# Optimization experiments

Measured on AMD Instinct MI355X. Metric: run time of the kernel, lower is better.

## Reference

```python
import jax, jax.numpy as jnp
import numpy as np

T, D_MODEL, D_FF, N_EXPERTS, TOP_K = 8192, 1024, 4096, 8, 2

def setup_inputs() -> dict:
    key = jax.random.key(0)
    k1, k2, k3, k4, k5 = jax.random.split(key, 5)
    hidden_states = jax.random.normal(k1, (T, D_MODEL), dtype=jnp.float32)
    # router picks TOP_K distinct-ish experts per token; build one-hot mask [T, K, E]
    expert_idx = jax.random.randint(k2, (T, TOP_K), 0, N_EXPERTS)
    selected_experts = jax.nn.one_hot(expert_idx, N_EXPERTS, dtype=jnp.int32)
    rw = jax.random.uniform(k3, (T, TOP_K), dtype=jnp.float32)
    routing_weights = rw / jnp.sum(rw, axis=-1, keepdims=True)
    scale = 1.0 / np.sqrt(D_MODEL)
    wi = jax.random.normal(k4, (N_EXPERTS, D_FF, D_MODEL), dtype=jnp.float32) * scale
    wo = jax.random.normal(k5, (N_EXPERTS, D_MODEL, D_FF), dtype=jnp.float32) * (1.0 / np.sqrt(D_FF))
    return {"hidden_states": hidden_states, "selected_experts": selected_experts,
            "routing_weights": routing_weights, "wi": wi, "wo": wo}

def reference(hidden_states, selected_experts, routing_weights, wi, wo):
    # expert_mask: [E, K, T] (as in torch permute(2,1,0))
    mask = jnp.transpose(selected_experts, (2, 1, 0)).astype(hidden_states.dtype)
    # combined per-token weight for each expert: w[t, e] = sum_k mask[e,k,t]*routing_weights[t,k]
    w = jnp.einsum('ekt,tk->te', mask, routing_weights)
    out = jnp.zeros_like(hidden_states)
    # fixed small loop over experts; tokens not routed to expert e get weight 0,
    # so this is mathematically identical to the gather->MLP->scale->scatter-add.
    for e in range(wi.shape[0]):
        h = jax.nn.relu(hidden_states @ wi[e].T)     # [T, d_ff] (dropout is identity at eval)
        y = h @ wo[e].T                              # [T, d_model]
        out = out + w[:, e:e + 1] * y
    return out
```

## Files before the change

kernel.cpp:

```cpp
#include <hip/hip_runtime.h>
#include <hip/hip_bf16.h>


#define T_TOK   8192
#define D_MODEL 1024
#define D_FF    4096
#define NE      8
#define MT2     72
#define ROWS_MAX (MT2 * 256)
#define BUFB    32768
#define LDS_G1  98304
#define BUF2    24576
#define LDS_G2  73728

typedef float f32x4 __attribute__((ext_vector_type(4)));
typedef short s16x8 __attribute__((ext_vector_type(8)));
typedef short s16x4 __attribute__((ext_vector_type(4)));
typedef unsigned short u16;

__device__ __forceinline__ u16 f2bf(float x) {
  __hip_bfloat16 h = __float2bfloat16(x);
  return *reinterpret_cast<u16*>(&h);
}

__device__ __forceinline__ s16x8 cvt8(float4 a, float4 b) {
  s16x8 v;
  v[0] = (short)f2bf(a.x); v[1] = (short)f2bf(a.y);
  v[2] = (short)f2bf(a.z); v[3] = (short)f2bf(a.w);
  v[4] = (short)f2bf(b.x); v[5] = (short)f2bf(b.y);
  v[6] = (short)f2bf(b.z); v[7] = (short)f2bf(b.w);
  return v;
}

__device__ __forceinline__ void gload_lds16(const void* g, void* l) {
  __builtin_amdgcn_global_load_lds((const __attribute__((address_space(1))) void*)g,
                                   (__attribute__((address_space(3))) void*)l,
                                   16, 0, 0);
}

__global__ void moe_route(const int* __restrict__ sel, const float* __restrict__ rw,
                          int* __restrict__ cnt, int* __restrict__ tidx,
                          float* __restrict__ tw) {
  int t = blockIdx.x * blockDim.x + threadIdx.x;
  if (t >= T_TOK) return;
  int e0 = 0, e1 = 0;
  #pragma unroll
  for (int e = 0; e < NE; ++e) {
    if (sel[t * 16 + e])     e0 = e;
    if (sel[t * 16 + 8 + e]) e1 = e;
  }
  float w0 = rw[2 * t], w1 = rw[2 * t + 1];
  if (e0 == e1) {
    int p = atomicAdd(&cnt[e0], 1);
    tidx[e0 * T_TOK + p] = t; tw[e0 * T_TOK + p] = w0 + w1;
  } else {
    int p = atomicAdd(&cnt[e0], 1);
    tidx[e0 * T_TOK + p] = t; tw[e0 * T_TOK + p] = w0;
    int q = atomicAdd(&cnt[e1], 1);
    tidx[e1 * T_TOK + q] = t; tw[e1 * T_TOK + q] = w1;
  }
}

__global__ void moe_tilemap(const int* __restrict__ cnt, const int* __restrict__ tidx,
                            const float* __restrict__ tw, int* __restrict__ te256,
                            int* __restrict__ tokr, float* __restrict__ wr) {
  int off[NE + 1];
  {
    int o = 0;
    #pragma unroll
    for (int e = 0; e < NE; ++e) { off[e] = o; o += (cnt[e] + 255) & ~255; }
    off[NE] = o;
  }
  const int total = off[NE];
  const int gid = blockIdx.x * blockDim.x + threadIdx.x;
  const int stride = gridDim.x * blockDim.x;
  for (int t = gid; t < MT2; t += stride) {
    int r0 = t * 256; int e = -1;
    if (r0 < total) {
      #pragma unroll
      for (int i = NE - 1; i >= 0; --i) if (r0 >= off[i]) { e = i; break; }
    }
    te256[t] = e;
  }
  for (int i = gid; i < ROWS_MAX; i += stride) {
    if (i >= total) { tokr[i] = -1; wr[i] = 0.f; continue; }
    int e = 0;
    #pragma unroll
    for (int k = NE - 1; k >= 0; --k) if (i >= off[k]) { e = k; break; }
    int j = i - off[e];
    int ok = j < cnt[e];
    tokr[i] = ok ? tidx[e * T_TOK + j] : -1;
    wr[i]   = ok ? tw[e * T_TOK + j] : 0.f;
  }
}

__global__ void moe_gather_x(const float* __restrict__ hs, const int* __restrict__ tokr,
                             u16* __restrict__ Xg) {
  int row = blockIdx.x;
  int tok = tokr[row];
  int c = threadIdx.x * 4;
  u16* dst = Xg + (size_t)row * D_MODEL + c;
  s16x4 o;
  if (tok < 0) {
    o[0] = o[1] = o[2] = o[3] = 0;
  } else {
    float4 v = *(const float4*)(hs + (size_t)tok * D_MODEL + c);
    o[0] = (short)f2bf(v.x); o[1] = (short)f2bf(v.y);
    o[2] = (short)f2bf(v.z); o[3] = (short)f2bf(v.w);
  }
  *(s16x4*)dst = o;
}

__global__ void moe_cvt_w(const float* __restrict__ wi, const float* __restrict__ wo,
                          u16* __restrict__ wib, u16* __restrict__ wob) {
  const size_t NW = (size_t)NE * D_FF * D_MODEL;
  size_t i = ((size_t)blockIdx.x * blockDim.x + threadIdx.x) * 8;
  const float* src; u16* dst;
  if (i < NW) { src = wi + i; dst = wib + i; }
  else        { src = wo + (i - NW); dst = wob + (i - NW); }
  float4 a = *(const float4*)(src);
  float4 b = *(const float4*)(src + 4);
  *(s16x8*)dst = cvt8(a, b);
}

__global__ void moe_cvt_wi_s(const float* __restrict__ wi, u16* __restrict__ wis,
                             int W, int f0) {
  size_t i = ((size_t)blockIdx.x * blockDim.x + threadIdx.x) * 8;
  size_t per = (size_t)W * D_MODEL;
  int e = (int)(i / per); size_t r = i % per;
  const float* src = wi + ((size_t)e * D_FF + f0) * D_MODEL + r;
  float4 a = *(const float4*)src;
  float4 b = *(const float4*)(src + 4);
  *(s16x8*)(wis + i) = cvt8(a, b);
}

__global__ void moe_cvt_wo_s(const float* __restrict__ wo, u16* __restrict__ wos,
                             int W, int f0) {
  size_t i = ((size_t)blockIdx.x * blockDim.x + threadIdx.x) * 8;
  size_t per = (size_t)D_MODEL * W;
  int e = (int)(i / per); size_t r = i % per;
  int row = (int)(r / W), col = (int)(r % W);
  const float* src = wo + ((size_t)e * D_MODEL + row) * D_FF + f0 + col;
  float4 a = *(const float4*)src;
  float4 b = *(const float4*)(src + 4);
  *(s16x8*)(wos + i) = cvt8(a, b);
}

template <bool FULL>
__global__ __launch_bounds__(512, 1)
void moe_g1(const u16* __restrict__ Xg, const u16* __restrict__ wiP,
            const int* __restrict__ te256, u16* __restrict__ H,
            int W, int f0) {
  extern __shared__ char lds[];
  const int GR = gridDim.x;
  const int task = (blockIdx.x & 7) * (GR >> 3) + (blockIdx.x >> 3);
  const int mt = task % MT2;
  const int nc = task / MT2;
  const int e = te256[mt];
  if (e < 0) return;
  const int grow0 = mt * 256;
  const int fcol = nc * 256;

  const int tid = threadIdx.x;
  const int lane = tid & 63, wv = tid >> 6;
  const int lg = lane >> 4, ll = lane & 15;
  const int wm = wv >> 2, wn = wv & 3;

  const int sw = (tid * 16) ^ (((tid >> 3) & 7) << 4);
  const int srow = sw >> 6, scol = sw & 63;
  const int inner = (ll * 64 + lg * 16) ^ (((ll >> 1) & 7) << 4);

  const char* gA = (const char*)(Xg + (size_t)grow0 * D_MODEL);
  const char* gB = (const char*)(wiP + (FULL ? ((size_t)e * D_FF + f0 + fcol)
                                             : ((size_t)e * W + fcol)) * D_MODEL);

  f32x4 acc[8][4];
  #pragma unroll
  for (int m = 0; m < 8; ++m)
    #pragma unroll
    for (int n = 0; n < 4; ++n) acc[m][n] = (f32x4){0.f, 0.f, 0.f, 0.f};

  auto stage = [&](int kb, char* lbuf) {
    #pragma unroll
    for (int j = 0; j < 2; ++j)
      gload_lds16(gA + (size_t)(j * 128 + srow) * 2048 + kb + scol,
                  lbuf + j * 8192 + tid * 16);
    #pragma unroll
    for (int j = 0; j < 2; ++j)
      gload_lds16(gB + (size_t)(j * 128 + srow) * 2048 + kb + scol,
                  lbuf + 16384 + j * 8192 + tid * 16);
  };

  const int NT = D_MODEL / 32;
  stage(0, lds);
  stage(64, lds + BUFB);
  int bufi = 0;
  for (int t = 0; t < NT; ++t) {
    if (t < NT - 1) { asm volatile("s_waitcnt vmcnt(4)" ::: "memory"); }
    else            { asm volatile("s_waitcnt vmcnt(0)" ::: "memory"); }
    asm volatile("s_barrier" ::: "memory");
    const char* la = lds + bufi * BUFB + wm * 8192;
    const char* lb = lds + bufi * BUFB + 16384 + wn * 4096;
    if (t + 2 < NT) {
      int b2 = bufi + 2; if (b2 >= 3) b2 -= 3;
      stage((t + 2) * 64, lds + b2 * BUFB);
    }
    s16x8 bq0 = *(const s16x8*)(lb + 0 * 1024 + inner);
    s16x8 bq1 = *(const s16x8*)(lb + 1 * 1024 + inner);
    s16x8 bq2 = *(const s16x8*)(lb + 2 * 1024 + inner);
    s16x8 bq3 = *(const s16x8*)(lb + 3 * 1024 + inner);
    {
      s16x8 a0 = *(const s16x8*)(la + 0 * 1024 + inner);
      s16x8 a1 = *(const s16x8*)(la + 1 * 1024 + inner);
      s16x8 a2 = *(const s16x8*)(la + 2 * 1024 + inner);
      s16x8 a3 = *(const s16x8*)(la + 3 * 1024 + inner);
      __builtin_amdgcn_s_setprio(1);
      acc[0][0] = __builtin_amdgcn_mfma_f32_16x16x32_bf16(a0, bq0, acc[0][0], 0, 0, 0);
      acc[0][1] = __builtin_amdgcn_mfma_f32_16x16x32_bf16(a0, bq1, acc[0][1], 0, 0, 0);
      acc[0][2] = __builtin_amdgcn_mfma_f32_16x16x32_bf16(a0, bq2, acc[0][2], 0, 0, 0);
      acc[0][3] = __builtin_amdgcn_mfma_f32_16x16x32_bf16(a0, bq3, acc[0][3], 0, 0, 0);
      acc[1][0] = __builtin_amdgcn_mfma_f32_16x16x32_bf16(a1, bq0, acc[1][0], 0, 0, 0);
      acc[1][1] = __builtin_amdgcn_mfma_f32_16x16x32_bf16(a1, bq1, acc[1][1], 0, 0, 0);
      acc[1][2] = __builtin_amdgcn_mfma_f32_16x16x32_bf16(a1, bq2, acc[1][2], 0, 0, 0);
      acc[1][3] = __builtin_amdgcn_mfma_f32_16x16x32_bf16(a1, bq3, acc[1][3], 0, 0, 0);
      acc[2][0] = __builtin_amdgcn_mfma_f32_16x16x32_bf16(a2, bq0, acc[2][0], 0, 0, 0);
      acc[2][1] = __builtin_amdgcn_mfma_f32_16x16x32_bf16(a2, bq1, acc[2][1], 0, 0, 0);
      acc[2][2] = __builtin_amdgcn_mfma_f32_16x16x32_bf16(a2, bq2, acc[2][2], 0, 0, 0);
      acc[2][3] = __builtin_amdgcn_mfma_f32_16x16x32_bf16(a2, bq3, acc[2][3], 0, 0, 0);
      acc[3][0] = __builtin_amdgcn_mfma_f32_16x16x32_bf16(a3, bq0, acc[3][0], 0, 0, 0);
      acc[3][1] = __builtin_amdgcn_mfma_f32_16x16x32_bf16(a3, bq1, acc[3][1], 0, 0, 0);
      acc[3][2] = __builtin_amdgcn_mfma_f32_16x16x32_bf16(a3, bq2, acc[3][2], 0, 0, 0);
      acc[3][3] = __builtin_amdgcn_mfma_f32_16x16x32_bf16(a3, bq3, acc[3][3], 0, 0, 0);
      __builtin_amdgcn_s_setprio(0);
    }
    __builtin_amdgcn_s_barrier();
    {
      s16x8 a0 = *(const s16x8*)(la + 4 * 1024 + inner);
      s16x8 a1 = *(const s16x8*)(la + 5 * 1024 + inner);
      s16x8 a2 = *(const s16x8*)(la + 6 * 1024 + inner);
      s16x8 a3 = *(const s16x8*)(la + 7 * 1024 + inner);
      __builtin_amdgcn_s_setprio(1);
      acc[4][0] = __builtin_amdgcn_mfma_f32_16x16x32_bf16(a0, bq0, acc[4][0], 0, 0, 0);
      acc[4][1] = __builtin_amdgcn_mfma_f32_16x16x32_bf16(a0, bq1, acc[4][1], 0, 0, 0);
      acc[4][2] = __builtin_amdgcn_mfma_f32_16x16x32_bf16(a0, bq2, acc[4][2], 0, 0, 0);
      acc[4][3] = __builtin_amdgcn_mfma_f32_16x16x32_bf16(a0, bq3, acc[4][3], 0, 0, 0);
      acc[5][0] = __builtin_amdgcn_mfma_f32_16x16x32_bf16(a1, bq0, acc[5][0], 0, 0, 0);
      acc[5][1] = __builtin_amdgcn_mfma_f32_16x16x32_bf16(a1, bq1, acc[5][1], 0, 0, 0);
      acc[5][2] = __builtin_amdgcn_mfma_f32_16x16x32_bf16(a1, bq2, acc[5][2], 0, 0, 0);
      acc[5][3] = __builtin_amdgcn_mfma_f32_16x16x32_bf16(a1, bq3, acc[5][3], 0, 0, 0);
      acc[6][0] = __builtin_amdgcn_mfma_f32_16x16x32_bf16(a2, bq0, acc[6][0], 0, 0, 0);
      acc[6][1] = __builtin_amdgcn_mfma_f32_16x16x32_bf16(a2, bq1, acc[6][1], 0, 0, 0);
      acc[6][2] = __builtin_amdgcn_mfma_f32_16x16x32_bf16(a2, bq2, acc[6][2], 0, 0, 0);
      acc[6][3] = __builtin_amdgcn_mfma_f32_16x16x32_bf16(a2, bq3, acc[6][3], 0, 0, 0);
      acc[7][0] = __builtin_amdgcn_mfma_f32_16x16x32_bf16(a3, bq0, acc[7][0], 0, 0, 0);
      acc[7][1] = __builtin_amdgcn_mfma_f32_16x16x32_bf16(a3, bq1, acc[7][1], 0, 0, 0);
      acc[7][2] = __builtin_amdgcn_mfma_f32_16x16x32_bf16(a3, bq2, acc[7][2], 0, 0, 0);
      acc[7][3] = __builtin_amdgcn_mfma_f32_16x16x32_bf16(a3, bq3, acc[7][3], 0, 0, 0);
      __builtin_amdgcn_s_setprio(0);
    }
    bufi += 1; if (bufi >= 3) bufi -= 3;
  }

  #pragma unroll
  for (int mf = 0; mf < 8; ++mf) {
    #pragma unroll
    for (int r = 0; r < 4; ++r) {
      int row = grow0 + wm * 128 + mf * 16 + lg * 4 + r;
      u16* hp = H + (size_t)row * W + fcol + wn * 64 + ll;
      #pragma unroll
      for (int nf = 0; nf < 4; ++nf) {
        float v = acc[mf][nf][r];
        hp[nf * 16] = f2bf(v > 0.f ? v : 0.f);
      }
    }
  }
}

template <bool FULL>
__global__ __launch_bounds__(512, 4)
void moe_g2(const u16* __restrict__ H, const u16* __restrict__ woP,
            const int* __restrict__ te256, const int* __restrict__ tokr,
            const float* __restrict__ wr, float* __restrict__ out,
            int W, int f0, int KCH) {
  extern __shared__ char lds[];
  const int GR = gridDim.x;
  const int task = (blockIdx.x & 7) * (GR >> 3) + (blockIdx.x >> 3);
  const int dc = task & 7;
  const int rest = task >> 3;
  const int mt = rest % MT2;
  const int kc = rest / MT2;
  const int e = te256[mt];
  if (e < 0) return;
  const int grow0 = mt * 256;
  const int dcol0 = dc * 128;

  const int tid = threadIdx.x;
  const int lane = tid & 63, wv = tid >> 6;
  const int lg = lane >> 4, ll = lane & 15;
  const int wm = wv >> 1, wn = wv & 1;

  const int sw = (tid * 16) ^ (((tid >> 3) & 7) << 4);
  const int srow = sw >> 6, scol = sw & 63;
  const int inner = (ll * 64 + lg * 16) ^ (((ll >> 1) & 7) << 4);

  const size_t pA = (size_t)W * 2;
  const size_t pB = (FULL ? (size_t)D_FF : (size_t)W) * 2;
  const char* gA = (const char*)(H + (size_t)grow0 * W) + (size_t)kc * KCH * 2;
  const char* gB = (const char*)(woP + ((size_t)e * D_MODEL + dcol0) * (pB / 2)
                                 + (FULL ? f0 : 0)) + (size_t)kc * KCH * 2;

  f32x4 acc[4][4];
  #pragma unroll
  for (int m = 0; m < 4; ++m)
    #pragma unroll
    for (int n = 0; n < 4; ++n) acc[m][n] = (f32x4){0.f, 0.f, 0.f, 0.f};

  auto stage = [&](int kb, char* lbuf) {
    #pragma unroll
    for (int j = 0; j < 2; ++j)
      gload_lds16(gA + (size_t)(j * 128 + srow) * pA + kb + scol,
                  lbuf + j * 8192 + tid * 16);
    {
      int brow = srow & 127;
      gload_lds16(gB + (size_t)brow * pB + kb + ((sw & 8191) & 63)
                  , lbuf + 16384 + (tid & 511) * 16);
    }
  };

  const int NT = KCH / 32;
  stage(0, lds);
  stage(64, lds + BUF2);
  int bufi = 0;
  for (int t = 0; t < NT; ++t) {
    if (t < NT - 1) { asm volatile("s_waitcnt vmcnt(3)" ::: "memory"); }
    else            { asm volatile("s_waitcnt vmcnt(0)" ::: "memory"); }
    asm volatile("s_barrier" ::: "memory");
    const char* la = lds + bufi * BUF2 + wm * 4096;
    const char* lb = lds + bufi * BUF2 + 16384 + wn * 4096;
    if (t + 2 < NT) {
      int b2 = bufi + 2; if (b2 >= 3) b2 -= 3;
      stage((t + 2) * 64, lds + b2 * BUF2);
    }
    s16x8 bq0 = *(const s16x8*)(lb + 0 * 1024 + inner);
    s16x8 bq1 = *(const s16x8*)(lb + 1 * 1024 + inner);
    s16x8 bq2 = *(const s16x8*)(lb + 2 * 1024 + inner);
    s16x8 bq3 = *(const s16x8*)(lb + 3 * 1024 + inner);
    s16x8 a0 = *(const s16x8*)(la + 0 * 1024 + inner);
    s16x8 a1 = *(const s16x8*)(la + 1 * 1024 + inner);
    s16x8 a2 = *(const s16x8*)(la + 2 * 1024 + inner);
    s16x8 a3 = *(const s16x8*)(la + 3 * 1024 + inner);
    __builtin_amdgcn_s_setprio(1);
    acc[0][0] = __builtin_amdgcn_mfma_f32_16x16x32_bf16(a0, bq0, acc[0][0], 0, 0, 0);
    acc[0][1] = __builtin_amdgcn_mfma_f32_16x16x32_bf16(a0, bq1, acc[0][1], 0, 0, 0);
    acc[0][2] = __builtin_amdgcn_mfma_f32_16x16x32_bf16(a0, bq2, acc[0][2], 0, 0, 0);
    acc[0][3] = __builtin_amdgcn_mfma_f32_16x16x32_bf16(a0, bq3, acc[0][3], 0, 0, 0);
    acc[1][0] = __builtin_amdgcn_mfma_f32_16x16x32_bf16(a1, bq0, acc[1][0], 0, 0, 0);
    acc[1][1] = __builtin_amdgcn_mfma_f32_16x16x32_bf16(a1, bq1, acc[1][1], 0, 0, 0);
    acc[1][2] = __builtin_amdgcn_mfma_f32_16x16x32_bf16(a1, bq2, acc[1][2], 0, 0, 0);
    acc[1][3] = __builtin_amdgcn_mfma_f32_16x16x32_bf16(a1, bq3, acc[1][3], 0, 0, 0);
    acc[2][0] = __builtin_amdgcn_mfma_f32_16x16x32_bf16(a2, bq0, acc[2][0], 0, 0, 0);
    acc[2][1] = __builtin_amdgcn_mfma_f32_16x16x32_bf16(a2, bq1, acc[2][1], 0, 0, 0);
    acc[2][2] = __builtin_amdgcn_mfma_f32_16x16x32_bf16(a2, bq2, acc[2][2], 0, 0, 0);
    acc[2][3] = __builtin_amdgcn_mfma_f32_16x16x32_bf16(a2, bq3, acc[2][3], 0, 0, 0);
    acc[3][0] = __builtin_amdgcn_mfma_f32_16x16x32_bf16(a3, bq0, acc[3][0], 0, 0, 0);
    acc[3][1] = __builtin_amdgcn_mfma_f32_16x16x32_bf16(a3, bq1, acc[3][1], 0, 0, 0);
    acc[3][2] = __builtin_amdgcn_mfma_f32_16x16x32_bf16(a3, bq2, acc[3][2], 0, 0, 0);
    acc[3][3] = __builtin_amdgcn_mfma_f32_16x16x32_bf16(a3, bq3, acc[3][3], 0, 0, 0);
    __builtin_amdgcn_s_setprio(0);
    bufi += 1; if (bufi >= 3) bufi -= 3;
  }

  #pragma unroll
  for (int mf = 0; mf < 4; ++mf) {
    #pragma unroll
    for (int r = 0; r < 4; ++r) {
      int row = grow0 + wm * 64 + mf * 16 + lg * 4 + r;
      int tok = tokr[row];
      if (tok >= 0) {
        float w = wr[row];
        float* op = out + (size_t)tok * D_MODEL + dcol0 + wn * 64 + ll;
        #pragma unroll
        for (int nf = 0; nf < 4; ++nf)
          atomicAdd(op + nf * 16, acc[mf][nf][r] * w);
      }
    }
  }
}

extern "C" void kernel_launch(void* const* d_in, const int* in_sizes, int n_in,
                              void* d_out, int out_size, void* d_ws, size_t ws_size,
                              hipStream_t stream) {
  const float* hs  = (const float*)d_in[0];
  const int*   sel = (const int*)d_in[1];
  const float* rw  = (const float*)d_in[2];
  const float* wi  = (const float*)d_in[3];
  const float* wo  = (const float*)d_in[4];
  float* out = (float*)d_out;

  const size_t NW   = (size_t)NE * D_FF * D_MODEL;
  const size_t CTRL = 1u << 20;
  const size_t WB   = 2 * NW * sizeof(u16);
  const size_t XGB  = (size_t)ROWS_MAX * D_MODEL * 2;

  bool FULLW = true; int W = D_FF;
  {
    bool found = false;
    for (int f : {1, 2, 4, 8, 16}) {
      int Wc = D_FF / f;
      size_t need = CTRL + WB + XGB + (size_t)ROWS_MAX * Wc * 2;
      if (need <= ws_size) { FULLW = true; W = Wc; found = true; break; }
    }
    if (!found) {
      for (int Wc : {1024, 512, 256}) {
        size_t sl = (size_t)2 * NE * Wc * D_MODEL * 2;
        size_t need = CTRL + sl + XGB + (size_t)ROWS_MAX * Wc * 2;
        if (need <= ws_size) { FULLW = false; W = Wc; break; }
      }
    }
  }
  const int FS = D_FF / W;

  size_t off = 0;
  auto take = [&](size_t b) -> char* {
    char* r = (char*)d_ws + off; off = (off + b + 255) & ~(size_t)255; return r;
  };
  int*   tidx = (int*)take((size_t)NE * T_TOK * 4);
  float* tw   = (float*)take((size_t)NE * T_TOK * 4);
  int*   tokr = (int*)take((size_t)ROWS_MAX * 4);
  float* wrr  = (float*)take((size_t)ROWS_MAX * 4);
  int*   te2  = (int*)take(MT2 * 4);
  int*   cnt  = (int*)take(256);
  off = CTRL;
  u16 *wiP, *woP;
  if (FULLW) { wiP = (u16*)take(NW * 2); woP = (u16*)take(NW * 2); }
  else       { wiP = (u16*)take((size_t)NE * W * D_MODEL * 2);
               woP = (u16*)take((size_t)NE * D_MODEL * W * 2); }
  u16* Xg   = (u16*)take(XGB);
  u16* Hbuf = (u16*)take((size_t)ROWS_MAX * W * 2);

  hipMemsetAsync(cnt, 0, 256, stream);
  hipMemsetAsync(d_out, 0, (size_t)out_size * sizeof(float), stream);
  moe_route<<<T_TOK / 256, 256, 0, stream>>>(sel, rw, cnt, tidx, tw);
  moe_tilemap<<<64, 256, 0, stream>>>(cnt, tidx, tw, te2, tokr, wrr);
  moe_gather_x<<<ROWS_MAX, 256, 0, stream>>>(hs, tokr, Xg);
  if (FULLW)
    moe_cvt_w<<<(int)(2 * NW / 8 / 256), 256, 0, stream>>>(wi, wo, wiP, woP);

  hipFuncSetAttribute(reinterpret_cast<const void*>(&moe_g1<true>),
                      hipFuncAttributeMaxDynamicSharedMemorySize, LDS_G1);
  hipFuncSetAttribute(reinterpret_cast<const void*>(&moe_g1<false>),
                      hipFuncAttributeMaxDynamicSharedMemorySize, LDS_G1);
  hipFuncSetAttribute(reinterpret_cast<const void*>(&moe_g2<true>),
                      hipFuncAttributeMaxDynamicSharedMemorySize, LDS_G2);
  hipFuncSetAttribute(reinterpret_cast<const void*>(&moe_g2<false>),
                      hipFuncAttributeMaxDynamicSharedMemorySize, LDS_G2);

  const int KCH = W / 2;
  const int g1grid = MT2 * (W / 256);
  const int g2grid = MT2 * 8 * 2;
  const int cvtblk = (int)(((size_t)NE * W * D_MODEL / 8) / 256);

  for (int p = 0; p < FS; ++p) {
    const int f0 = p * W;
    if (!FULLW) {
      moe_cvt_wi_s<<<cvtblk, 256, 0, stream>>>(wi, wiP, W, f0);
      moe_cvt_wo_s<<<cvtblk, 256, 0, stream>>>(wo, woP, W, f0);
    }
    if (FULLW) {
      moe_g1<true><<<g1grid, 512, LDS_G1, stream>>>(Xg, wiP, te2, Hbuf, W, f0);
      moe_g2<true><<<g2grid, 512, LDS_G2, stream>>>(Hbuf, woP, te2, tokr, wrr,
                                                    out, W, f0, KCH);
    } else {
      moe_g1<false><<<g1grid, 512, LDS_G1, stream>>>(Xg, wiP, te2, Hbuf, W, f0);
      moe_g2<false><<<g2grid, 512, LDS_G2, stream>>>(Hbuf, woP, te2, tokr, wrr,
                                                     out, W, f0, KCH);
    }
  }
}
```

Measured before the change: 537.1 us.

## Switch MoE GEMMs to double-buffered LDS and retune occupancy

Both expert GEMM kernels move from a three-buffer LDS ring, where the next stage is issued before compute, to two buffers where the prefetch two steps ahead is issued into the just-consumed buffer after a trailing barrier. This shrinks LDS per block so the first GEMM can target two blocks per CU. The second GEMM's occupancy target drops from four to three and its B-tile load addressing is simplified. The mid-iteration barrier in the first GEMM is removed. In exchange, the load-issue slot moves later in each iteration, and two blocks per CU for a 128-accumulator kernel raises register-pressure and spill risk.

```diff
diff --git a/kernel.cpp b/kernel.cpp
--- a/kernel.cpp
+++ b/kernel.cpp
@@ -8,10 +8,10 @@
 #define NE      8
 #define MT2     72
 #define ROWS_MAX (MT2 * 256)
-#define BUFB    32768
-#define LDS_G1  98304
+#define BUF1    32768
+#define LDS_G1  65536
 #define BUF2    24576
-#define LDS_G2  73728
+#define LDS_G2  49152
 
 typedef float f32x4 __attribute__((ext_vector_type(4)));
 typedef short s16x8 __attribute__((ext_vector_type(8)));
@@ -146,8 +146,14 @@
   *(s16x8*)(wos + i) = cvt8(a, b);
 }
 
+#define MM4(mi, a) \
+  acc[mi][0] = __builtin_amdgcn_mfma_f32_16x16x32_bf16(a, bq0, acc[mi][0], 0, 0, 0); \
+  acc[mi][1] = __builtin_amdgcn_mfma_f32_16x16x32_bf16(a, bq1, acc[mi][1], 0, 0, 0); \
+  acc[mi][2] = __builtin_amdgcn_mfma_f32_16x16x32_bf16(a, bq2, acc[mi][2], 0, 0, 0); \
+  acc[mi][3] = __builtin_amdgcn_mfma_f32_16x16x32_bf16(a, bq3, acc[mi][3], 0, 0, 0);
+
 template <bool FULL>
-__global__ __launch_bounds__(512, 1)
+__global__ __launch_bounds__(512, 2)
 void moe_g1(const u16* __restrict__ Xg, const u16* __restrict__ wiP,
             const int* __restrict__ te256, u16* __restrict__ H,
             int W, int f0) {
@@ -193,18 +199,14 @@
 
   const int NT = D_MODEL / 32;
   stage(0, lds);
-  stage(64, lds + BUFB);
-  int bufi = 0;
+  stage(64, lds + BUF1);
   for (int t = 0; t < NT; ++t) {
     if (t < NT - 1) { asm volatile("s_waitcnt vmcnt(4)" ::: "memory"); }
     else            { asm volatile("s_waitcnt vmcnt(0)" ::: "memory"); }
     asm volatile("s_barrier" ::: "memory");
-    const char* la = lds + bufi * BUFB + wm * 8192;
-    const char* lb = lds + bufi * BUFB + 16384 + wn * 4096;
-    if (t + 2 < NT) {
-      int b2 = bufi + 2; if (b2 >= 3) b2 -= 3;
-      stage((t + 2) * 64, lds + b2 * BUFB);
-    }
+    char* lbuf = lds + (t & 1) * BUF1;
+    const char* la = lbuf + wm * 8192;
+    const char* lb = lbuf + 16384 + wn * 4096;
     s16x8 bq0 = *(const s16x8*)(lb + 0 * 1024 + inner);
     s16x8 bq1 = *(const s16x8*)(lb + 1 * 1024 + inner);
     s16x8 bq2 = *(const s16x8*)(lb + 2 * 1024 + inner);
@@ -215,50 +217,20 @@
       s16x8 a2 = *(const s16x8*)(la + 2 * 1024 + inner);
       s16x8 a3 = *(const s16x8*)(la + 3 * 1024 + inner);
       __builtin_amdgcn_s_setprio(1);
-      acc[0][0] = __builtin_amdgcn_mfma_f32_16x16x32_bf16(a0, bq0, acc[0][0], 0, 0, 0);
-      acc[0][1] = __builtin_amdgcn_mfma_f32_16x16x32_bf16(a0, bq1, acc[0][1], 0, 0, 0);
-      acc[0][2] = __builtin_amdgcn_mfma_f32_16x16x32_bf16(a0, bq2, acc[0][2], 0, 0, 0);
-      acc[0][3] = __builtin_amdgcn_mfma_f32_16x16x32_bf16(a0, bq3, acc[0][3], 0, 0, 0);
-      acc[1][0] = __builtin_amdgcn_mfma_f32_16x16x32_bf16(a1, bq0, acc[1][0], 0, 0, 0);
-      acc[1][1] = __builtin_amdgcn_mfma_f32_16x16x32_bf16(a1, bq1, acc[1][1], 0, 0, 0);
-      acc[1][2] = __builtin_amdgcn_mfma_f32_16x16x32_bf16(a1, bq2, acc[1][2], 0, 0, 0);
-      acc[1][3] = __builtin_amdgcn_mfma_f32_16x16x32_bf16(a1, bq3, acc[1][3], 0, 0, 0);
-      acc[2][0] = __builtin_amdgcn_mfma_f32_16x16x32_bf16(a2, bq0, acc[2][0], 0, 0, 0);
-      acc[2][1] = __builtin_amdgcn_mfma_f32_16x16x32_bf16(a2, bq1, acc[2][1], 0, 0, 0);
-      acc[2][2] = __builtin_amdgcn_mfma_f32_16x16x32_bf16(a2, bq2, acc[2][2], 0, 0, 0);
-      acc[2][3] = __builtin_amdgcn_mfma_f32_16x16x32_bf16(a2, bq3, acc[2][3], 0, 0, 0);
-      acc[3][0] = __builtin_amdgcn_mfma_f32_16x16x32_bf16(a3, bq0, acc[3][0], 0, 0, 0);
-      acc[3][1] = __builtin_amdgcn_mfma_f32_16x16x32_bf16(a3, bq1, acc[3][1], 0, 0, 0);
-      acc[3][2] = __builtin_amdgcn_mfma_f32_16x16x32_bf16(a3, bq2, acc[3][2], 0, 0, 0);
-      acc[3][3] = __builtin_amdgcn_mfma_f32_16x16x32_bf16(a3, bq3, acc[3][3], 0, 0, 0);
+      MM4(0, a0) MM4(1, a1) MM4(2, a2) MM4(3, a3)
       __builtin_amdgcn_s_setprio(0);
     }
-    __builtin_amdgcn_s_barrier();
     {
       s16x8 a0 = *(const s16x8*)(la + 4 * 1024 + inner);
       s16x8 a1 = *(const s16x8*)(la + 5 * 1024 + inner);
       s16x8 a2 = *(const s16x8*)(la + 6 * 1024 + inner);
       s16x8 a3 = *(const s16x8*)(la + 7 * 1024 + inner);
       __builtin_amdgcn_s_setprio(1);
-      acc[4][0] = __builtin_amdgcn_mfma_f32_16x16x32_bf16(a0, bq0, acc[4][0], 0, 0, 0);
-      acc[4][1] = __builtin_amdgcn_mfma_f32_16x16x32_bf16(a0, bq1, acc[4][1], 0, 0, 0);
-      acc[4][2] = __builtin_amdgcn_mfma_f32_16x16x32_bf16(a0, bq2, acc[4][2], 0, 0, 0);
-      acc[4][3] = __builtin_amdgcn_mfma_f32_16x16x32_bf16(a0, bq3, acc[4][3], 0, 0, 0);
-      acc[5][0] = __builtin_amdgcn_mfma_f32_16x16x32_bf16(a1, bq0, acc[5][0], 0, 0, 0);
-      acc[5][1] = __builtin_amdgcn_mfma_f32_16x16x32_bf16(a1, bq1, acc[5][1], 0, 0, 0);
-      acc[5][2] = __builtin_amdgcn_mfma_f32_16x16x32_bf16(a1, bq2, acc[5][2], 0, 0, 0);
-      acc[5][3] = __builtin_amdgcn_mfma_f32_16x16x32_bf16(a1, bq3, acc[5][3], 0, 0, 0);
-      acc[6][0] = __builtin_amdgcn_mfma_f32_16x16x32_bf16(a2, bq0, acc[6][0], 0, 0, 0);
-      acc[6][1] = __builtin_amdgcn_mfma_f32_16x16x32_bf16(a2, bq1, acc[6][1], 0, 0, 0);
-      acc[6][2] = __builtin_amdgcn_mfma_f32_16x16x32_bf16(a2, bq2, acc[6][2], 0, 0, 0);
-      acc[6][3] = __builtin_amdgcn_mfma_f32_16x16x32_bf16(a2, bq3, acc[6][3], 0, 0, 0);
-      acc[7][0] = __builtin_amdgcn_mfma_f32_16x16x32_bf16(a3, bq0, acc[7][0], 0, 0, 0);
-      acc[7][1] = __builtin_amdgcn_mfma_f32_16x16x32_bf16(a3, bq1, acc[7][1], 0, 0, 0);
-      acc[7][2] = __builtin_amdgcn_mfma_f32_16x16x32_bf16(a3, bq2, acc[7][2], 0, 0, 0);
-      acc[7][3] = __builtin_amdgcn_mfma_f32_16x16x32_bf16(a3, bq3, acc[7][3], 0, 0, 0);
+      MM4(4, a0) MM4(5, a1) MM4(6, a2) MM4(7, a3)
       __builtin_amdgcn_s_setprio(0);
     }
-    bufi += 1; if (bufi >= 3) bufi -= 3;
+    asm volatile("s_barrier" ::: "memory");
+    if (t + 2 < NT) stage((t + 2) * 64, lbuf);
   }
 
   #pragma unroll
@@ -277,7 +249,7 @@
 }
 
 template <bool FULL>
-__global__ __launch_bounds__(512, 4)
+__global__ __launch_bounds__(512, 3)
 void moe_g2(const u16* __restrict__ H, const u16* __restrict__ woP,
             const int* __restrict__ te256, const int* __restrict__ tokr,
             const float* __restrict__ wr, float* __restrict__ out,
@@ -320,54 +292,39 @@
     for (int j = 0; j < 2; ++j)
       gload_lds16(gA + (size_t)(j * 128 + srow) * pA + kb + scol,
                   lbuf + j * 8192 + tid * 16);
-    {
-      int brow = srow & 127;
-      gload_lds16(gB + (size_t)brow * pB + kb + ((sw & 8191) & 63)
-                  , lbuf + 16384 + (tid & 511) * 16);
-    }
+    gload_lds16(gB + (size_t)srow * pB + kb + scol, lbuf + 16384 + tid * 16);
   };
 
   const int NT = KCH / 32;
   stage(0, lds);
   stage(64, lds + BUF2);
-  int bufi = 0;
   for (int t = 0; t < NT; ++t) {
     if (t < NT - 1) { asm volatile("s_waitcnt vmcnt(3)" ::: "memory"); }
     else            { asm volatile("s_waitcnt vmcnt(0)" ::: "memory"); }
     asm volatile("s_barrier" ::: "memory");
-    const char* la = lds + bufi * BUF2 + wm * 4096;
-    const char* lb = lds + bufi * BUF2 + 16384 + wn * 4096;
-    if (t + 2 < NT) {
-      int b2 = bufi + 2; if (b2 >= 3) b2 -= 3;
-      stage((t + 2) * 64, lds + b2 * BUF2);
-    }
+    char* lbuf = lds + (t & 1) * BUF2;
+    const char* la = lbuf + wm * 4096;
+    const char* lb = lbuf + 16384 + wn * 4096;
     s16x8 bq0 = *(const s16x8*)(lb + 0 * 1024 + inner);
     s16x8 bq1 = *(const s16x8*)(lb + 1 * 1024 + inner);
     s16x8 bq2 = *(const s16x8*)(lb + 2 * 1024 + inner);
     s16x8 bq3 = *(const s16x8*)(lb + 3 * 1024 + inner);
-    s16x8 a0 = *(const s16x8*)(la + 0 * 1024 + inner);
-    s16x8 a1 = *(const s16x8*)(la + 1 * 1024 + inner);
-    s16x8 a2 = *(const s16x8*)(la + 2 * 1024 + inner);
-    s16x8 a3 = *(const s16x8*)(la + 3 * 1024 + inner);
-    __builtin_amdgcn_s_setprio(1);
-    acc[0][0] = __builtin_amdgcn_mfma_f32_16x16x32_bf16(a0, bq0, acc[0][0], 0, 0, 0);
-    acc[0][1] = __builtin_amdgcn_mfma_f32_16x16x32_bf16(a0, bq1, acc[0][1], 0, 0, 0);
-    acc[0][2] = __builtin_amdgcn_mfma_f32_16x16x32_bf16(a0, bq2, acc[0][2], 0, 0, 0);
-    acc[0][3] = __builtin_amdgcn_mfma_f32_16x16x32_bf16(a0, bq3, acc[0][3], 0, 0, 0);
-    acc[1][0] = __builtin_amdgcn_mfma_f32_16x16x32_bf16(a1, bq0, acc[1][0], 0, 0, 0);
-    acc[1][1] = __builtin_amdgcn_mfma_f32_16x16x32_bf16(a1, bq1, acc[1][1], 0, 0, 0);
-    acc[1][2] = __builtin_amdgcn_mfma_f32_16x16x32_bf16(a1, bq2, acc[1][2], 0, 0, 0);
-    acc[1][3] = __builtin_amdgcn_mfma_f32_16x16x32_bf16(a1, bq3, acc[1][3], 0, 0, 0);
-    acc[2][0] = __builtin_amdgcn_mfma_f32_16x16x32_bf16(a2, bq0, acc[2][0], 0, 0, 0);
-    acc[2][1] = __builtin_amdgcn_mfma_f32_16x16x32_bf16(a2, bq1, acc[2][1], 0, 0, 0);
-    acc[2][2] = __builtin_amdgcn_mfma_f32_16x16x32_bf16(a2, bq2, acc[2][2], 0, 0, 0);
-    acc[2][3] = __builtin_amdgcn_mfma_f32_16x16x32_bf16(a2, bq3, acc[2][3], 0, 0, 0);
-    acc[3][0] = __builtin_amdgcn_mfma_f32_16x16x32_bf16(a3, bq0, acc[3][0], 0, 0, 0);
-    acc[3][1] = __builtin_amdgcn_mfma_f32_16x16x32_bf16(a3, bq1, acc[3][1], 0, 0, 0);
-    acc[3][2] = __builtin_amdgcn_mfma_f32_16x16x32_bf16(a3, bq2, acc[3][2], 0, 0, 0);
-    acc[3][3] = __builtin_amdgcn_mfma_f32_16x16x32_bf16(a3, bq3, acc[3][3], 0, 0, 0);
-    __builtin_amdgcn_s_setprio(0);
-    bufi += 1; if (bufi >= 3) bufi -= 3;
+    {
+      s16x8 a0 = *(const s16x8*)(la + 0 * 1024 + inner);
+      s16x8 a1 = *(const s16x8*)(la + 1 * 1024 + inner);
+      __builtin_amdgcn_s_setprio(1);
+      MM4(0, a0) MM4(1, a1)
+      __builtin_amdgcn_s_setprio(0);
+    }
+    {
+      s16x8 a2 = *(const s16x8*)(la + 2 * 1024 + inner);
+      s16x8 a3 = *(const s16x8*)(la + 3 * 1024 + inner);
+      __builtin_amdgcn_s_setprio(1);
+      MM4(2, a2) MM4(3, a3)
+      __builtin_amdgcn_s_setprio(0);
+    }
+    asm volatile("s_barrier" ::: "memory");
+    if (t + 2 < NT) stage((t + 2) * 64, lbuf);
   }
 
   #pragma unroll
```

After: 557.2 us. +3.7%, slower.
